# Kernel optimization log

Hardware: AMD Instinct MI355X
Metric: run time of the kernel (lower is better)

## Reference

```python
import jax, jax.numpy as jnp
import numpy as np

B, N, L, H, D, IN = 512, 128, 10, 16, 8, 16
NT = B * N
E = NT * 16

def _lin(key, fan_in, shape):
    b = 1.0 / np.sqrt(fan_in)
    return jax.random.uniform(key, shape, jnp.float32, -b, b)

def setup_inputs() -> dict:
    key = jax.random.key(0)
    ks = jax.random.split(key, 12)
    x = jax.random.normal(ks[0], (NT, IN), jnp.float32)
    # within-graph random edges so to_dense_adj is well defined
    g = jax.random.randint(ks[1], (E,), 0, B)
    i = jax.random.randint(ks[2], (E,), 0, N)
    j = jax.random.randint(ks[3], (E,), 0, N)
    edge_index = jnp.stack([g * N + i, g * N + j]).astype(jnp.int32)
    return dict(
        x=x,
        gin_w1=_lin(ks[4], H, (2, L, H, H)),   # [ld/ud, layer, H, H]
        gin_b1=_lin(ks[5], H, (2, L, H)),
        gin_w2=_lin(ks[6], H, (2, L, H, H)),
        gin_b2=_lin(ks[7], H, (2, L, H)),
        mean_w=_lin(ks[8], H, (2, H, D)),
        mean_b=jnp.zeros((2, D), jnp.float32),
        std_w=_lin(ks[9], H, (2, H, D)),
        std_b=jnp.zeros((2, D), jnp.float32),
        edge_index=edge_index,
    )

def _encoder(x, w1, b1, w2, b2, mw, mb, sw, sb, src, dst):
    # PyG GIN stack: GINConv(MLP[Lin->ReLU->Lin]), eps=0, sum aggregation,
    # ReLU between layers (dropout = identity in eval mode).
    h = x
    for l in range(L):
        agg = jax.ops.segment_sum(h[src], dst, num_segments=NT)
        t = h + agg  # (1+eps)*x + sum_{j in N(i)} x_j with eps=0
        t = jnp.maximum(t @ w1[l] + b1[l], 0.0) @ w2[l] + b2[l]
        h = jnp.maximum(t, 0.0) if l < L - 1 else t
    mean = h @ mw + mb
    std = jax.nn.softplus(h @ sw + sb)
    return mean, std

def reference(x, gin_w1, gin_b1, gin_w2, gin_b2, mean_w, mean_b, std_w, std_b, edge_index):
    src, dst = edge_index[0], edge_index[1]
    enc = jax.vmap(_encoder, in_axes=(None, 0, 0, 0, 0, 0, 0, 0, 0, None, None))
    mean, std = enc(x, gin_w1, gin_b1, gin_w2, gin_b2,
                    mean_w, mean_b, std_w, std_b, src, dst)  # [2, NT, D]
    # reparameterized sample: eps ~ N(0,1) (prior.sample, detached)
    eps = jax.random.normal(jax.random.key(42), (2, NT, D), jnp.float32)
    z = mean + std * eps
    z_ld = z[0].reshape(B, N, D)
    z_ud = z[1].reshape(B, N, D)
    logits = jnp.einsum('bnd,bmd->bnm', z_ld, z_ud)  # per-graph inner-product decode
    dense_adj = jnp.zeros((B, N, N), jnp.float32).at[src // N, src % N, dst % N].add(1.0)
    n_pos = dense_adj.sum()
    posw = (B * N * N - n_pos) / n_pos
    # BCE-with-logits, pos_weight, reduction='sum'
    nll = jnp.sum(posw * dense_adj * jax.nn.softplus(-logits)
                  + (1.0 - dense_adj) * jax.nn.softplus(logits))
    # KL(N(mean,std) || N(0,1)), summed over both encoders
    kl = jnp.sum(-jnp.log(std) + 0.5 * (std * std + mean * mean) - 0.5)
    return nll, kl, jax.nn.sigmoid(logits), dense_adj
```

## Files before the change

kernel.cpp:

```cpp
#include <hip/hip_runtime.h>

#define B_    512
#define N_    128
#define L_    10
#define H_    16
#define D_    8
#define NT_   65536
#define E_    1048576
#define NNB_  8388608
#define CAP_  4096
#define CCAP_ 2816
#define HS_   20

__device__ __forceinline__ unsigned rotl32(unsigned v, int r){ return (v<<r)|(v>>(32-r)); }

__device__ __forceinline__ void threefry2x32(unsigned c0, unsigned c1, unsigned &o0, unsigned &o1){
  const unsigned ks0 = 0u, ks1 = 42u, ks2 = 0u ^ 42u ^ 0x1BD11BDAu;
  unsigned x0 = c0 + ks0, x1 = c1 + ks1;
#define TFR(r) { x0 += x1; x1 = rotl32(x1, r); x1 ^= x0; }
  TFR(13) TFR(15) TFR(26) TFR(6)   x0 += ks1; x1 += ks2 + 1u;
  TFR(17) TFR(29) TFR(16) TFR(24)  x0 += ks2; x1 += ks0 + 2u;
  TFR(13) TFR(15) TFR(26) TFR(6)   x0 += ks0; x1 += ks1 + 3u;
  TFR(17) TFR(29) TFR(16) TFR(24)  x0 += ks1; x1 += ks2 + 4u;
  TFR(13) TFR(15) TFR(26) TFR(6)   x0 += ks2; x1 += ks0 + 5u;
#undef TFR
  o0 = x0; o1 = x1;
}

__device__ __forceinline__ float erfinv_f(float x){
  float w = -log1pf(-x*x);
  float p;
  if (w < 5.0f) {
    w -= 2.5f;
    p = 2.81022636e-08f;
    p = fmaf(p, w, 3.43273939e-07f);
    p = fmaf(p, w, -3.5233877e-06f);
    p = fmaf(p, w, -4.39150654e-06f);
    p = fmaf(p, w, 0.00021858087f);
    p = fmaf(p, w, -0.00125372503f);
    p = fmaf(p, w, -0.00417768164f);
    p = fmaf(p, w, 0.246640727f);
    p = fmaf(p, w, 1.50140941f);
  } else {
    w = sqrtf(w) - 3.0f;
    p = -0.000200214257f;
    p = fmaf(p, w, 0.000100950558f);
    p = fmaf(p, w, 0.00134934322f);
    p = fmaf(p, w, -0.00367342844f);
    p = fmaf(p, w, 0.00573950773f);
    p = fmaf(p, w, -0.0076224613f);
    p = fmaf(p, w, 0.00943887047f);
    p = fmaf(p, w, 1.00167406f);
    p = fmaf(p, w, 2.83297682f);
  }
  return p * x;
}

__device__ __forceinline__ float softplus_f(float x){
  return fmaxf(x, 0.0f) + log1pf(expf(-fabsf(x)));
}

__device__ __forceinline__ void blockReduceAdd(double v, double* target){
  __shared__ double red[4];
  int lane = threadIdx.x & 63;
  int w    = threadIdx.x >> 6;
  #pragma unroll
  for(int off = 32; off > 0; off >>= 1) v += __shfl_down(v, off);
  if(lane == 0) red[w] = v;
  __syncthreads();
  if(threadIdx.x == 0){
    double s = red[0];
    int nw = (blockDim.x + 63) >> 6;
    for(int k = 1; k < nw; k++) s += red[k];
    atomicAdd(target, s);
  }
}

__global__ __launch_bounds__(256)
void k_bin(const int* __restrict__ ei, int* __restrict__ gcount,
           unsigned short* __restrict__ ebuf){
  __shared__ int cnt[512];
  __shared__ int gb[512];
  const int t = threadIdx.x;
  cnt[t] = 0; cnt[t + 256] = 0;
  __syncthreads();
  int kv[8];
  const int base = blockIdx.x * 2048;
  #pragma unroll
  for(int q = 0; q < 8; q++){
    int e = base + q*256 + t;
    int s = ei[e];
    int d = ei[E_ + e];
    int g = d >> 7;
    kv[q] = (g << 14) | ((s & 127) << 7) | (d & 127);
    atomicAdd(&cnt[g], 1);
  }
  __syncthreads();
  #pragma unroll
  for(int g = 0; g < 512; g += 256){
    int c = cnt[g + t];
    gb[g + t] = c ? atomicAdd(&gcount[g + t], c) : 0;
    cnt[g + t] = 0;
  }
  __syncthreads();
  #pragma unroll
  for(int q = 0; q < 8; q++){
    int g = kv[q] >> 14;
    int pos = atomicAdd(&cnt[g], 1);
    int idx = gb[g] + pos;
    if(idx < CAP_) ebuf[(size_t)g*CAP_ + idx] = (unsigned short)(kv[q] & 0x3FFF);
  }
}

__global__ __launch_bounds__(128)
void k_csr(const unsigned short* __restrict__ ebuf, const int* __restrict__ gcount,
           unsigned short* __restrict__ gcol, int* __restrict__ grow){
  __shared__ int cnt[128], off[128], sc[128];
  const int b = blockIdx.x, t = threadIdx.x;
  int ec = gcount[b]; if(ec > CAP_) ec = CAP_;
  const unsigned short* eb = ebuf + (size_t)b*CAP_;
  cnt[t] = 0;
  __syncthreads();
  for(int q = t; q < ec; q += 128) atomicAdd(&cnt[eb[q] & 127], 1);
  __syncthreads();
  int pdeg = (cnt[t] + 3) & ~3;
  sc[t] = pdeg;
  __syncthreads();
  for(int o = 1; o < 128; o <<= 1){
    int v = (t >= o) ? sc[t - o] : 0;
    __syncthreads();
    sc[t] += v;
    __syncthreads();
  }
  off[t] = sc[t] - pdeg;
  grow[b*129 + t] = off[t];
  if(t == 127) grow[b*129 + 128] = sc[127];
  cnt[t] = 0;
  __syncthreads();
  {
    uint4 s128; s128.x = s128.y = s128.z = s128.w = 0x00800080u;
    uint4* g4 = (uint4*)(gcol + (size_t)b*CCAP_);
    #pragma unroll
    for(int k = 0; k < 3; k++){ int q = t + 128*k; if(q < CCAP_/8) g4[q] = s128; }
  }
  __syncthreads();
  for(int q = t; q < ec; q += 128){
    int pk = eb[q];
    int d = pk & 127;
    int pos = atomicAdd(&cnt[d], 1);
    int idx = off[d] + pos;
    if(idx < CCAP_) gcol[(size_t)b*CCAP_ + idx] = (unsigned short)(pk >> 7);
  }
}

__global__ __launch_bounds__(128, 4)
void k_mega(const float* __restrict__ x, const unsigned short* __restrict__ gcol,
            const int* __restrict__ grow,
            const float* __restrict__ gw1, const float* __restrict__ gb1,
            const float* __restrict__ gw2, const float* __restrict__ gb2,
            const float* __restrict__ mw,  const float* __restrict__ mb,
            const float* __restrict__ sw,  const float* __restrict__ sb,
            float* __restrict__ z, double* acc){
  __shared__ __align__(16) float hh[129*HS_ + 4];
  __shared__ __align__(16) unsigned short col_l[CCAP_];
  const int b = blockIdx.x, e = blockIdx.y, t = threadIdx.x;

  {
    const float4* x4 = (const float4*)x + (size_t)b*512;
    #pragma unroll
    for(int k = 0; k < 4; k++){
      int q = t + 128*k;
      float4 v = x4[q];
      *(float4*)&hh[(q >> 2)*HS_ + (q & 3)*4] = v;
    }
    if(t < 16) hh[128*HS_ + t] = 0.0f;
  }
  {
    const uint4* gc4 = (const uint4*)(gcol + (size_t)b*CCAP_);
    uint4* cl4 = (uint4*)col_l;
    #pragma unroll
    for(int k = 0; k < 3; k++){ int q = t + 128*k; if(q < CCAP_/8) cl4[q] = gc4[q]; }
  }
  const int r0 = grow[b*129 + t], r1 = grow[b*129 + t + 1];
  __syncthreads();

  const float* w1g = gw1 + e*(L_*256);
  const float* w2g = gw2 + e*(L_*256);
  const float* b1g = gb1 + e*(L_*16);
  const float* b2g = gb2 + e*(L_*16);

  for(int l = 0; l < L_; l++){
    float ag[16];
    {
      const float4* hp = (const float4*)&hh[t*HS_];
      float4 s0 = hp[0], s1 = hp[1], s2 = hp[2], s3 = hp[3];
      ag[0]=s0.x; ag[1]=s0.y; ag[2]=s0.z; ag[3]=s0.w;
      ag[4]=s1.x; ag[5]=s1.y; ag[6]=s1.z; ag[7]=s1.w;
      ag[8]=s2.x; ag[9]=s2.y; ag[10]=s2.z; ag[11]=s2.w;
      ag[12]=s3.x; ag[13]=s3.y; ag[14]=s3.z; ag[15]=s3.w;
    }
    for(int r = r0; r < r1; r += 4){
      ushort4 c4 = *(const ushort4*)&col_l[r];
      const float4* n0 = (const float4*)&hh[c4.x*HS_];
      const float4* n1 = (const float4*)&hh[c4.y*HS_];
      const float4* n2 = (const float4*)&hh[c4.z*HS_];
      const float4* n3 = (const float4*)&hh[c4.w*HS_];
      #pragma unroll
      for(int c = 0; c < 4; c++){
        float4 v0 = n0[c], v1 = n1[c], v2 = n2[c], v3 = n3[c];
        ag[c*4+0] += v0.x + v1.x + v2.x + v3.x;
        ag[c*4+1] += v0.y + v1.y + v2.y + v3.y;
        ag[c*4+2] += v0.z + v1.z + v2.z + v3.z;
        ag[c*4+3] += v0.w + v1.w + v2.w + v3.w;
      }
    }
    float u[16];
    #pragma unroll
    for(int j = 0; j < 16; j++){
      float s = b1g[l*16 + j];
      #pragma unroll
      for(int k = 0; k < 16; k++) s = fmaf(ag[k], w1g[l*256 + k*16 + j], s);
      u[j] = fmaxf(s, 0.0f);
    }
    float ov[16];
    #pragma unroll
    for(int c = 0; c < 16; c++){
      float s = b2g[l*16 + c];
      #pragma unroll
      for(int k = 0; k < 16; k++) s = fmaf(u[k], w2g[l*256 + k*16 + c], s);
      ov[c] = (l < L_-1) ? fmaxf(s, 0.0f) : s;
    }
    __syncthreads();
    {
      float4* hw = (float4*)&hh[t*HS_];
      hw[0] = make_float4(ov[0], ov[1], ov[2], ov[3]);
      hw[1] = make_float4(ov[4], ov[5], ov[6], ov[7]);
      hw[2] = make_float4(ov[8], ov[9], ov[10], ov[11]);
      hw[3] = make_float4(ov[12], ov[13], ov[14], ov[15]);
    }
    __syncthreads();
  }

  float hv[16];
  {
    const float4* hp = (const float4*)&hh[t*HS_];
    float4 a0 = hp[0], a1 = hp[1], a2 = hp[2], a3 = hp[3];
    hv[0]=a0.x; hv[1]=a0.y; hv[2]=a0.z; hv[3]=a0.w;
    hv[4]=a1.x; hv[5]=a1.y; hv[6]=a1.z; hv[7]=a1.w;
    hv[8]=a2.x; hv[9]=a2.y; hv[10]=a2.z; hv[11]=a2.w;
    hv[12]=a3.x; hv[13]=a3.y; hv[14]=a3.z; hv[15]=a3.w;
  }
  const float* mwg = mw + e*128; const float* mbg = mb + e*8;
  const float* swg = sw + e*128; const float* sbg = sb + e*8;
  double kll = 0.0;
  float zv[8];
  unsigned fbase = ((unsigned)e*NT_ + (unsigned)(b*128 + t))*8u;
  #pragma unroll
  for(int d = 0; d < 8; d++){
    float mm = mbg[d], ss = sbg[d];
    #pragma unroll
    for(int k = 0; k < 16; k++){
      mm = fmaf(hv[k], mwg[k*8 + d], mm);
      ss = fmaf(hv[k], swg[k*8 + d], ss);
    }
    float stdv = softplus_f(ss);
    unsigned o0, o1; threefry2x32(0u, fbase + d, o0, o1);
    unsigned bits = o0 ^ o1;
    float uu = __uint_as_float((bits >> 9) | 0x3f800000u) - 1.0f;
    const float lo = -0.99999994f;
    float uval = fmaxf(lo, fmaf(uu, 2.0f, lo));
    float eps = 1.41421356f * erfinv_f(uval);
    zv[d] = mm + stdv * eps;
    float stdc = fmaxf(stdv, 1e-37f);
    float term = 0.5f*(stdv*stdv + mm*mm) - logf(stdc) - 0.5f;
    if(!(term == term) || term > 1e30f) term = 1e30f;
    kll += (double)term;
  }
  {
    float4* zp = (float4*)(z + (size_t)fbase);
    zp[0] = make_float4(zv[0], zv[1], zv[2], zv[3]);
    zp[1] = make_float4(zv[4], zv[5], zv[6], zv[7]);
  }
  blockReduceAdd(kll, acc + 1);
}

#define TSB_ 132
__global__ __launch_bounds__(256, 4)
void k_decode(const float* __restrict__ z, const unsigned short* __restrict__ ebuf,
              const int* __restrict__ gcount, float* __restrict__ sig,
              float* __restrict__ adj, double* acc){
  __shared__ float zl[1024];
  __shared__ float zu[1152];
  __shared__ unsigned tile32[128*TSB_/4];
  const int b = blockIdx.x, t = threadIdx.x;
  const float* zld = z + (size_t)b*1024;
  const float* zud = z + (size_t)NT_*8 + (size_t)b*1024;
  for(int k = t; k < 1024; k += 256){
    zl[k] = zld[k];
    zu[(k >> 3)*9 + (k & 7)] = zud[k];
  }
  {
    uint4 zz; zz.x = zz.y = zz.z = zz.w = 0u;
    uint4* t4 = (uint4*)tile32;
    for(int k = t; k < 128*TSB_/16; k += 256) t4[k] = zz;
  }
  __syncthreads();
  {
    int ec = gcount[b]; if(ec > CAP_) ec = CAP_;
    const unsigned short* eb = ebuf + (size_t)b*CAP_;
    for(int q = t; q < ec; q += 256){
      int pk = eb[q];
      int cell = (pk >> 7)*TSB_ + (pk & 127);
      atomicAdd(&tile32[cell >> 2], 1u << ((cell & 3)*8));
    }
  }
  __syncthreads();
  double local = 0.0;
  float* sigb = sig + (size_t)b*16384;
  float* adjb = adj + (size_t)b*16384;
  for(int it = 0; it < 16; it++){
    int base = it*1024 + t*4;
    int n = base >> 7, mcol = base & 127;
    const float* za = &zl[n*8];
    float xs[4];
    #pragma unroll
    for(int c = 0; c < 4; c++){
      const float* zb = &zu[(mcol + c)*9];
      float xx = 0.0f;
      #pragma unroll
      for(int d = 0; d < 8; d++) xx = fmaf(za[d], zb[d], xx);
      xs[c] = xx;
    }
    unsigned packed = tile32[(n*TSB_ + mcol) >> 2];
    float4 av;
    av.x = (float)( packed        & 0xFF);
    av.y = (float)((packed >> 8)  & 0xFF);
    av.z = (float)((packed >> 16) & 0xFF);
    av.w = (float)((packed >> 24) & 0xFF);
    float ads[4] = {av.x, av.y, av.z, av.w};
    float sgs[4];
    #pragma unroll
    for(int c = 0; c < 4; c++){
      float xx = xs[c];
      sgs[c] = 1.0f / (1.0f + expf(-xx));
      float cc  = log1pf(expf(-fabsf(xx)));
      float spp = fmaxf(xx, 0.0f) + cc;
      float spn = fmaxf(-xx, 0.0f) + cc;
      local += (double)(7.0f*ads[c]*spn + (1.0f - ads[c])*spp);
    }
    ((float4*)(sigb + base))[0] = make_float4(sgs[0], sgs[1], sgs[2], sgs[3]);
    ((float4*)(adjb + base))[0] = av;
  }
  blockReduceAdd(local, acc + 0);
}

__device__ __forceinline__ float clamp_finite(double v){
  if(v != v) return 0.0f;
  if(v >  3.3e38) return  3.3e38f;
  if(v < -3.3e38) return -3.3e38f;
  return (float)v;
}
__global__ void k_final(const double* __restrict__ acc, float* __restrict__ out){
  if(threadIdx.x == 0){
    out[0] = clamp_finite(acc[0]);
    out[1] = clamp_finite(acc[1]);
  }
}

extern "C" void kernel_launch(void* const* d_in, const int* in_sizes, int n_in,
                              void* d_out, int out_size, void* d_ws, size_t ws_size,
                              hipStream_t stream){
  const float* x   = (const float*)d_in[0];
  const float* gw1 = (const float*)d_in[1];
  const float* gb1 = (const float*)d_in[2];
  const float* gw2 = (const float*)d_in[3];
  const float* gb2 = (const float*)d_in[4];
  const float* mw  = (const float*)d_in[5];
  const float* mb  = (const float*)d_in[6];
  const float* sw  = (const float*)d_in[7];
  const float* sb  = (const float*)d_in[8];
  const int*   ei  = (const int*)d_in[9];

  float* out = (float*)d_out;
  float* sig = out + 2;
  float* adj = out + 2 + NNB_;

  char* ws = (char*)d_ws;
  int*            gcount = (int*)(ws);
  double*         acc    = (double*)(ws + 2048);
  unsigned short* ebuf   = (unsigned short*)(ws + 4096);
  unsigned short* gcol   = (unsigned short*)(ws + 4096 + 2*512*CAP_);
  int*            grow   = (int*)(ws + 4096 + 2*512*CAP_ + 2*512*CCAP_);
  float*          z      = (float*)(ws + 4096 + 2*512*CAP_ + 2*512*CCAP_ + 4*512*132);

  hipMemsetAsync(ws, 0, 4096, stream);

  k_bin   <<<E_/2048, 256, 0, stream>>>(ei, gcount, ebuf);
  k_csr   <<<B_, 128, 0, stream>>>(ebuf, gcount, gcol, grow);
  k_mega  <<<dim3(B_, 2), 128, 0, stream>>>(x, gcol, grow, gw1, gb1, gw2, gb2,
                                            mw, mb, sw, sb, z, acc);
  k_decode<<<B_, 256, 0, stream>>>(z, ebuf, gcount, sig, adj, acc);
  k_final <<<1, 64, 0, stream>>>(acc, out);
}
```

Measured before the change: 240.2 us.

## Split each node across two threads in GIN megakernel with shuffle exchange

The GIN encoder kernel now uses 256 threads per graph, with two threads per node. Each thread aggregates and computes half of the 16 hidden features, and the halves are exchanged with xor-shuffles before each MLP layer. The head is split the same way, so each thread produces 4 of the 8 latent dims. This doubles thread-level parallelism and cuts per-thread registers and serial gather work, at the cost of more shuffles and redundant full-vector MLP inputs per thread.

```diff
diff --git a/kernel.cpp b/kernel.cpp
--- a/kernel.cpp
+++ b/kernel.cpp
@@ -153,7 +153,7 @@
   }
 }
 
-__global__ __launch_bounds__(128, 4)
+__global__ __launch_bounds__(256, 4)
 void k_mega(const float* __restrict__ x, const unsigned short* __restrict__ gcol,
             const int* __restrict__ grow,
             const float* __restrict__ gw1, const float* __restrict__ gb1,
@@ -164,12 +164,13 @@
   __shared__ __align__(16) float hh[129*HS_ + 4];
   __shared__ __align__(16) unsigned short col_l[CCAP_];
   const int b = blockIdx.x, e = blockIdx.y, t = threadIdx.x;
+  const int i = t >> 1, p = t & 1;
 
   {
     const float4* x4 = (const float4*)x + (size_t)b*512;
     #pragma unroll
-    for(int k = 0; k < 4; k++){
-      int q = t + 128*k;
+    for(int k = 0; k < 2; k++){
+      int q = t + 256*k;
       float4 v = x4[q];
       *(float4*)&hh[(q >> 2)*HS_ + (q & 3)*4] = v;
     }
@@ -179,98 +180,148 @@
     const uint4* gc4 = (const uint4*)(gcol + (size_t)b*CCAP_);
     uint4* cl4 = (uint4*)col_l;
     #pragma unroll
-    for(int k = 0; k < 3; k++){ int q = t + 128*k; if(q < CCAP_/8) cl4[q] = gc4[q]; }
-  }
-  const int r0 = grow[b*129 + t], r1 = grow[b*129 + t + 1];
-  __syncthreads();
-
-  const float* w1g = gw1 + e*(L_*256);
-  const float* w2g = gw2 + e*(L_*256);
-  const float* b1g = gb1 + e*(L_*16);
-  const float* b2g = gb2 + e*(L_*16);
+    for(int k = 0; k < 2; k++){ int q = t + 256*k; if(q < CCAP_/8) cl4[q] = gc4[q]; }
+  }
+  const int r0 = grow[b*129 + i], r1 = grow[b*129 + i + 1];
+  __syncthreads();
+
+  const float* w1g = gw1 + e*(L_*256) + p*8;
+  const float* w2g = gw2 + e*(L_*256) + p*8;
+  const float* b1g = gb1 + e*(L_*16) + p*8;
+  const float* b2g = gb2 + e*(L_*16) + p*8;
 
   for(int l = 0; l < L_; l++){
-    float ag[16];
+    float a[8];
     {
-      const float4* hp = (const float4*)&hh[t*HS_];
-      float4 s0 = hp[0], s1 = hp[1], s2 = hp[2], s3 = hp[3];
-      ag[0]=s0.x; ag[1]=s0.y; ag[2]=s0.z; ag[3]=s0.w;
-      ag[4]=s1.x; ag[5]=s1.y; ag[6]=s1.z; ag[7]=s1.w;
-      ag[8]=s2.x; ag[9]=s2.y; ag[10]=s2.z; ag[11]=s2.w;
-      ag[12]=s3.x; ag[13]=s3.y; ag[14]=s3.z; ag[15]=s3.w;
+      const float4* hp = (const float4*)&hh[i*HS_ + p*8];
+      float4 s0 = hp[0], s1 = hp[1];
+      a[0]=s0.x; a[1]=s0.y; a[2]=s0.z; a[3]=s0.w;
+      a[4]=s1.x; a[5]=s1.y; a[6]=s1.z; a[7]=s1.w;
     }
     for(int r = r0; r < r1; r += 4){
       ushort4 c4 = *(const ushort4*)&col_l[r];
-      const float4* n0 = (const float4*)&hh[c4.x*HS_];
-      const float4* n1 = (const float4*)&hh[c4.y*HS_];
-      const float4* n2 = (const float4*)&hh[c4.z*HS_];
-      const float4* n3 = (const float4*)&hh[c4.w*HS_];
+      const float4* n0 = (const float4*)&hh[c4.x*HS_ + p*8];
+      const float4* n1 = (const float4*)&hh[c4.y*HS_ + p*8];
+      const float4* n2 = (const float4*)&hh[c4.z*HS_ + p*8];
+      const float4* n3 = (const float4*)&hh[c4.w*HS_ + p*8];
       #pragma unroll
-      for(int c = 0; c < 4; c++){
+      for(int c = 0; c < 2; c++){
         float4 v0 = n0[c], v1 = n1[c], v2 = n2[c], v3 = n3[c];
-        ag[c*4+0] += v0.x + v1.x + v2.x + v3.x;
-        ag[c*4+1] += v0.y + v1.y + v2.y + v3.y;
-        ag[c*4+2] += v0.z + v1.z + v2.z + v3.z;
-        ag[c*4+3] += v0.w + v1.w + v2.w + v3.w;
+        a[c*4+0] += v0.x + v1.x + v2.x + v3.x;
+        a[c*4+1] += v0.y + v1.y + v2.y + v3.y;
+        a[c*4+2] += v0.z + v1.z + v2.z + v3.z;
+        a[c*4+3] += v0.w + v1.w + v2.w + v3.w;
       }
     }
-    float u[16];
-    #pragma unroll
-    for(int j = 0; j < 16; j++){
-      float s = b1g[l*16 + j];
+    float ag[16];
+    #pragma unroll
+    for(int q = 0; q < 8; q++){
+      float o = __shfl_xor(a[q], 1);
+      ag[q]     = p ? o    : a[q];
+      ag[q + 8] = p ? a[q] : o;
+    }
+    float u[8];
+    {
+      float s0 = 0, s1 = 0, s2 = 0, s3 = 0, s4 = 0, s5 = 0, s6 = 0, s7 = 0;
+      const float* wl = w1g + l*256;
       #pragma unroll
-      for(int k = 0; k < 16; k++) s = fmaf(ag[k], w1g[l*256 + k*16 + j], s);
-      u[j] = fmaxf(s, 0.0f);
-    }
-    float ov[16];
-    #pragma unroll
-    for(int c = 0; c < 16; c++){
-      float s = b2g[l*16 + c];
+      for(int k = 0; k < 16; k++){
+        const float4* wr = (const float4*)(wl + k*16);
+        float4 wa = wr[0], wb = wr[1];
+        float av = ag[k];
+        s0 = fmaf(av, wa.x, s0); s1 = fmaf(av, wa.y, s1);
+        s2 = fmaf(av, wa.z, s2); s3 = fmaf(av, wa.w, s3);
+        s4 = fmaf(av, wb.x, s4); s5 = fmaf(av, wb.y, s5);
+        s6 = fmaf(av, wb.z, s6); s7 = fmaf(av, wb.w, s7);
+      }
+      const float4* bb = (const float4*)(b1g + l*16);
+      float4 b0 = bb[0], b1v = bb[1];
+      u[0]=fmaxf(s0+b0.x,0.f); u[1]=fmaxf(s1+b0.y,0.f);
+      u[2]=fmaxf(s2+b0.z,0.f); u[3]=fmaxf(s3+b0.w,0.f);
+      u[4]=fmaxf(s4+b1v.x,0.f); u[5]=fmaxf(s5+b1v.y,0.f);
+      u[6]=fmaxf(s6+b1v.z,0.f); u[7]=fmaxf(s7+b1v.w,0.f);
+    }
+    float u16[16];
+    #pragma unroll
+    for(int q = 0; q < 8; q++){
+      float o = __shfl_xor(u[q], 1);
+      u16[q]     = p ? o    : u[q];
+      u16[q + 8] = p ? u[q] : o;
+    }
+    float ov[8];
+    {
+      float s0 = 0, s1 = 0, s2 = 0, s3 = 0, s4 = 0, s5 = 0, s6 = 0, s7 = 0;
+      const float* wl = w2g + l*256;
       #pragma unroll
-      for(int k = 0; k < 16; k++) s = fmaf(u[k], w2g[l*256 + k*16 + c], s);
-      ov[c] = (l < L_-1) ? fmaxf(s, 0.0f) : s;
+      for(int k = 0; k < 16; k++){
+        const float4* wr = (const float4*)(wl + k*16);
+        float4 wa = wr[0], wb = wr[1];
+        float uv = u16[k];
+        s0 = fmaf(uv, wa.x, s0); s1 = fmaf(uv, wa.y, s1);
+        s2 = fmaf(uv, wa.z, s2); s3 = fmaf(uv, wa.w, s3);
+        s4 = fmaf(uv, wb.x, s4); s5 = fmaf(uv, wb.y, s5);
+        s6 = fmaf(uv, wb.z, s6); s7 = fmaf(uv, wb.w, s7);
+      }
+      const float4* bb = (const float4*)(b2g + l*16);
+      float4 b0 = bb[0], b1v = bb[1];
+      ov[0]=s0+b0.x; ov[1]=s1+b0.y; ov[2]=s2+b0.z; ov[3]=s3+b0.w;
+      ov[4]=s4+b1v.x; ov[5]=s5+b1v.y; ov[6]=s6+b1v.z; ov[7]=s7+b1v.w;
+      if(l < L_-1){
+        #pragma unroll
+        for(int q = 0; q < 8; q++) ov[q] = fmaxf(ov[q], 0.0f);
+      }
     }
     __syncthreads();
     {
-      float4* hw = (float4*)&hh[t*HS_];
+      float4* hw = (float4*)&hh[i*HS_ + p*8];
       hw[0] = make_float4(ov[0], ov[1], ov[2], ov[3]);
       hw[1] = make_float4(ov[4], ov[5], ov[6], ov[7]);
-      hw[2] = make_float4(ov[8], ov[9], ov[10], ov[11]);
-      hw[3] = make_float4(ov[12], ov[13], ov[14], ov[15]);
     }
     __syncthreads();
   }
 
   float hv[16];
   {
-    const float4* hp = (const float4*)&hh[t*HS_];
+    const float4* hp = (const float4*)&hh[i*HS_];
     float4 a0 = hp[0], a1 = hp[1], a2 = hp[2], a3 = hp[3];
     hv[0]=a0.x; hv[1]=a0.y; hv[2]=a0.z; hv[3]=a0.w;
     hv[4]=a1.x; hv[5]=a1.y; hv[6]=a1.z; hv[7]=a1.w;
     hv[8]=a2.x; hv[9]=a2.y; hv[10]=a2.z; hv[11]=a2.w;
     hv[12]=a3.x; hv[13]=a3.y; hv[14]=a3.z; hv[15]=a3.w;
   }
-  const float* mwg = mw + e*128; const float* mbg = mb + e*8;
-  const float* swg = sw + e*128; const float* sbg = sb + e*8;
+  const float* mwg = mw + e*128 + p*4; const float* mbg = mb + e*8 + p*4;
+  const float* swg = sw + e*128 + p*4; const float* sbg = sb + e*8 + p*4;
   double kll = 0.0;
-  float zv[8];
-  unsigned fbase = ((unsigned)e*NT_ + (unsigned)(b*128 + t))*8u;
+  float zv[4];
+  unsigned fbase = ((unsigned)e*NT_ + (unsigned)(b*128 + i))*8u + (unsigned)(p*4);
+  float mmv[4], ssv[4];
+  {
+    float4 m4 = *(const float4*)mbg;
+    float4 s4 = *(const float4*)sbg;
+    mmv[0]=m4.x; mmv[1]=m4.y; mmv[2]=m4.z; mmv[3]=m4.w;
+    ssv[0]=s4.x; ssv[1]=s4.y; ssv[2]=s4.z; ssv[3]=s4.w;
+    #pragma unroll
+    for(int k = 0; k < 16; k++){
+      float4 mw4 = *(const float4*)(mwg + k*8);
+      float4 sw4 = *(const float4*)(swg + k*8);
+      float hk = hv[k];
+      mmv[0]=fmaf(hk, mw4.x, mmv[0]); mmv[1]=fmaf(hk, mw4.y, mmv[1]);
+      mmv[2]=fmaf(hk, mw4.z, mmv[2]); mmv[3]=fmaf(hk, mw4.w, mmv[3]);
+      ssv[0]=fmaf(hk, sw4.x, ssv[0]); ssv[1]=fmaf(hk, sw4.y, ssv[1]);
+      ssv[2]=fmaf(hk, sw4.z, ssv[2]); ssv[3]=fmaf(hk, sw4.w, ssv[3]);
+    }
+  }
   #pragma unroll
-  for(int d = 0; d < 8; d++){
-    float mm = mbg[d], ss = sbg[d];
-    #pragma unroll
-    for(int k = 0; k < 16; k++){
-      mm = fmaf(hv[k], mwg[k*8 + d], mm);
-      ss = fmaf(hv[k], swg[k*8 + d], ss);
-    }
+  for(int dd = 0; dd < 4; dd++){
+    float mm = mmv[dd], ss = ssv[dd];
     float stdv = softplus_f(ss);
-    unsigned o0, o1; threefry2x32(0u, fbase + d, o0, o1);
+    unsigned o0, o1; threefry2x32(0u, fbase + dd, o0, o1);
     unsigned bits = o0 ^ o1;
     float uu = __uint_as_float((bits >> 9) | 0x3f800000u) - 1.0f;
     const float lo = -0.99999994f;
     float uval = fmaxf(lo, fmaf(uu, 2.0f, lo));
     float eps = 1.41421356f * erfinv_f(uval);
-    zv[d] = mm + stdv * eps;
+    zv[dd] = mm + stdv * eps;
     float stdc = fmaxf(stdv, 1e-37f);
     float term = 0.5f*(stdv*stdv + mm*mm) - logf(stdc) - 0.5f;
     if(!(term == term) || term > 1e30f) term = 1e30f;
@@ -279,7 +330,6 @@
   {
     float4* zp = (float4*)(z + (size_t)fbase);
     zp[0] = make_float4(zv[0], zv[1], zv[2], zv[3]);
-    zp[1] = make_float4(zv[4], zv[5], zv[6], zv[7]);
   }
   blockReduceAdd(kll, acc + 1);
 }
@@ -397,7 +447,7 @@
 
   k_bin   <<<E_/2048, 256, 0, stream>>>(ei, gcount, ebuf);
   k_csr   <<<B_, 128, 0, stream>>>(ebuf, gcount, gcol, grow);
-  k_mega  <<<dim3(B_, 2), 128, 0, stream>>>(x, gcol, grow, gw1, gb1, gw2, gb2,
+  k_mega  <<<dim3(B_, 2), 256, 0, stream>>>(x, gcol, grow, gw1, gb1, gw2, gb2,
                                             mw, mb, sw, sb, z, acc);
   k_decode<<<B_, 256, 0, stream>>>(z, ebuf, gcount, sig, adj, acc);
   k_final <<<1, 64, 0, stream>>>(acc, out);
```

New measurement: 291.0 us. +21.2%, slower.
